# Kernel tuning notes

Measured on AMD Instinct MI355X. Metric: run time of the kernel, lower is better.

The kernel has to match this reference:

```python
import jax, jax.numpy as jnp
import numpy as np

N = 100000      # nodes
E = 1600000     # message-passing edges
P = 1000000     # prediction edges
DIN = 128       # node_in_channels
H = 128         # hidden_channels
DOUT = 64       # out_channels (node embedding)
EIN = 32        # edge_in_channels
EPS = 1e-5


def setup_inputs() -> dict:
    key = jax.random.key(0)
    ks = iter(jax.random.split(key, 48))
    nk = lambda: next(ks)
    rn = lambda shape: jax.random.normal(nk(), shape, dtype=jnp.float32)
    glorot = lambda shape: rn(shape) * (1.0 / np.sqrt(shape[-1]))
    inp = {
        "x": rn((N, DIN)),
        "edge_index": jax.random.randint(nk(), (2, E), 0, N),
        "pred_edge_index": jax.random.randint(nk(), (2, P), 0, N),
        "edge_features": rn((P, EIN)),
        # SAGEConv layer 1: lin_l (aggregated, with bias), lin_r (root, no bias)
        "sage1_Wl": glorot((H, DIN)), "sage1_bl": jnp.zeros((H,), jnp.float32), "sage1_Wr": glorot((H, DIN)),
        "bn1_g": jnp.ones((H,), jnp.float32), "bn1_b": jnp.zeros((H,), jnp.float32),
        "bn1_m": rn((H,)) * 0.1, "bn1_v": jnp.ones((H,), jnp.float32),
        # SAGEConv layer 2
        "sage2_Wl": glorot((DOUT, H)), "sage2_bl": jnp.zeros((DOUT,), jnp.float32), "sage2_Wr": glorot((DOUT, H)),
        # edge MLP: Linear(EIN, H//2) -> BN -> ReLU -> Linear(H//2, H//4)
        "edge_W1": glorot((H // 2, EIN)), "edge_b1": jnp.zeros((H // 2,), jnp.float32),
        "ebn_g": jnp.ones((H // 2,), jnp.float32), "ebn_b": jnp.zeros((H // 2,), jnp.float32),
        "ebn_m": rn((H // 2,)) * 0.1, "ebn_v": jnp.ones((H // 2,), jnp.float32),
        "edge_W2": glorot((H // 4, H // 2)), "edge_b2": jnp.zeros((H // 4,), jnp.float32),
        # predictor: Linear(2*DOUT+H//4, H) -> BN -> ReLU -> Linear(H, H//2) -> BN -> ReLU -> Linear(H//2, 1)
        "p_W1": glorot((H, 2 * DOUT + H // 4)), "p_b1": jnp.zeros((H,), jnp.float32),
        "pbn1_g": jnp.ones((H,), jnp.float32), "pbn1_b": jnp.zeros((H,), jnp.float32),
        "pbn1_m": rn((H,)) * 0.1, "pbn1_v": jnp.ones((H,), jnp.float32),
        "p_W2": glorot((H // 2, H)), "p_b2": jnp.zeros((H // 2,), jnp.float32),
        "pbn2_g": jnp.ones((H // 2,), jnp.float32), "pbn2_b": jnp.zeros((H // 2,), jnp.float32),
        "pbn2_m": rn((H // 2,)) * 0.1, "pbn2_v": jnp.ones((H // 2,), jnp.float32),
        "p_W3": glorot((1, H // 2)), "p_b3": jnp.zeros((1,), jnp.float32),
    }
    return inp


def _bn(h, g, b, m, v):
    # eval-mode BatchNorm1d with running stats
    return (h - m) * (g / jnp.sqrt(v + EPS)) + b


def _sage(h, src, dst, Wl, bl, Wr):
    # PyG SAGEConv (mean aggr): lin_l(mean of h[src] at dst) + lin_r(h)
    msg = jax.ops.segment_sum(h[src], dst, num_segments=N)        # [N, d]
    cnt = jax.ops.segment_sum(jnp.ones((src.shape[0],), h.dtype), dst, num_segments=N)
    agg = msg / jnp.maximum(cnt, 1.0)[:, None]
    return agg @ Wl.T + bl + h @ Wr.T


def reference(x, edge_index, pred_edge_index, edge_features,
              sage1_Wl, sage1_bl, sage1_Wr, bn1_g, bn1_b, bn1_m, bn1_v,
              sage2_Wl, sage2_bl, sage2_Wr,
              edge_W1, edge_b1, ebn_g, ebn_b, ebn_m, ebn_v, edge_W2, edge_b2,
              p_W1, p_b1, pbn1_g, pbn1_b, pbn1_m, pbn1_v,
              p_W2, p_b2, pbn2_g, pbn2_b, pbn2_m, pbn2_v, p_W3, p_b3):
    src, dst = edge_index[0], edge_index[1]
    # GraphSAGE encoder (eval mode: dropout off, BN running stats)
    h = _sage(x, src, dst, sage1_Wl, sage1_bl, sage1_Wr)
    h = jax.nn.relu(_bn(h, bn1_g, bn1_b, bn1_m, bn1_v))
    z = _sage(h, src, dst, sage2_Wl, sage2_bl, sage2_Wr)          # [N, DOUT]
    # edge-pair gather + concat
    combined = jnp.concatenate([z[pred_edge_index[0]], z[pred_edge_index[1]]], axis=-1)  # [P, 2*DOUT]
    # edge feature MLP
    e = edge_features @ edge_W1.T + edge_b1
    e = jax.nn.relu(_bn(e, ebn_g, ebn_b, ebn_m, ebn_v))
    e = e @ edge_W2.T + edge_b2                                   # [P, H//4]
    combined = jnp.concatenate([combined, e], axis=-1)            # [P, 2*DOUT + H//4]
    # predictor MLP
    u = combined @ p_W1.T + p_b1
    u = jax.nn.relu(_bn(u, pbn1_g, pbn1_b, pbn1_m, pbn1_v))
    u = u @ p_W2.T + p_b2
    u = jax.nn.relu(_bn(u, pbn2_g, pbn2_b, pbn2_m, pbn2_v))
    out = u @ p_W3.T + p_b3                                       # [P, 1]
    return out[:, 0]
```

## Files before the change

### kernel.cpp

```cpp
#include <hip/hip_runtime.h>

#define Nn 100000
#define Ee 1600000
#define Pp 1000000
#define EPSf 1e-5f

typedef _Float16 f16x8 __attribute__((ext_vector_type(8)));
typedef _Float16 f16x4 __attribute__((ext_vector_type(4)));
typedef _Float16 f16x2 __attribute__((ext_vector_type(2)));
typedef float f32x4 __attribute__((ext_vector_type(4)));

__device__ __forceinline__ float4 ld4(const float* p) { return *(const float4*)p; }

#define oW1l 0
#define oW1r 16384
#define oW2l 32768
#define oW2r 40960
#define oW1a 49152
#define oW1b 57344
#define oW1c 65536
#define oWe1 69632
#define oWe2 71680
#define oWp2 73728
#define W16_TOTAL 81920

#define BN_TOTAL 608

__global__ __launch_bounds__(256) void prep_kernel(
    const float* __restrict__ x,
    const float* __restrict__ s1Wl, const float* __restrict__ s1Wr,
    const float* __restrict__ s2Wl, const float* __restrict__ s2Wr,
    const float* __restrict__ pW1,  const float* __restrict__ eW1,
    const float* __restrict__ eW2,  const float* __restrict__ pW2,
    const float* __restrict__ eb1,
    const float* __restrict__ ebng, const float* __restrict__ ebnb,
    const float* __restrict__ ebnm, const float* __restrict__ ebnv,
    const float* __restrict__ eb2,
    const float* __restrict__ pb1,
    const float* __restrict__ p1g, const float* __restrict__ p1b,
    const float* __restrict__ p1m, const float* __restrict__ p1v,
    const float* __restrict__ pb2,
    const float* __restrict__ p2g, const float* __restrict__ p2b,
    const float* __restrict__ p2m, const float* __restrict__ p2v,
    const float* __restrict__ pW3,
    _Float16* __restrict__ w16, float* __restrict__ bnA,
    _Float16* __restrict__ x16) {
    int tid = blockIdx.x * 256 + threadIdx.x;
    if (tid < W16_TOTAL) {
        float v;
        if (tid < 16384)      v = s1Wl[tid];
        else if (tid < 32768) v = s1Wr[tid - 16384];
        else if (tid < 40960) v = s2Wl[tid - 32768];
        else if (tid < 49152) v = s2Wr[tid - 40960];
        else if (tid < 57344) { int l = tid - 49152; v = pW1[(l >> 6) * 160 + (l & 63)]; }
        else if (tid < 65536) { int l = tid - 57344; v = pW1[(l >> 6) * 160 + 64 + (l & 63)]; }
        else if (tid < 69632) { int l = tid - 65536; v = pW1[(l >> 5) * 160 + 128 + (l & 31)]; }
        else if (tid < 71680) v = eW1[tid - 69632];
        else if (tid < 73728) v = eW2[tid - 71680];
        else                  v = pW2[tid - 73728];
        w16[tid] = (_Float16)v;
    } else if (tid < W16_TOTAL + BN_TOTAL) {
        int b = tid - W16_TOTAL;
        float v;
        if (b < 64)       v = ebng[b] * rsqrtf(ebnv[b] + EPSf);
        else if (b < 128) { int c = b - 64;  float s = ebng[c] * rsqrtf(ebnv[c] + EPSf);
                            v = (eb1[c] - ebnm[c]) * s + ebnb[c]; }
        else if (b < 256) { int c = b - 128; v = p1g[c] * rsqrtf(p1v[c] + EPSf); }
        else if (b < 384) { int c = b - 256; float s = p1g[c] * rsqrtf(p1v[c] + EPSf);
                            v = (pb1[c] - p1m[c]) * s + p1b[c]; }
        else if (b < 448) { int c = b - 384; v = p2g[c] * rsqrtf(p2v[c] + EPSf); }
        else if (b < 512) { int c = b - 448; float s = p2g[c] * rsqrtf(p2v[c] + EPSf);
                            v = (pb2[c] - p2m[c]) * s + p2b[c]; }
        else if (b < 544) v = eb2[b - 512];
        else              v = pW3[b - 544];
        bnA[b] = v;
    }
    int stride = gridDim.x * 256;
    const int NV = Nn * 128 / 4;
    for (int i = tid; i < NV; i += stride) {
        float4 v = ((const float4*)x)[i];
        f16x4 h = {(_Float16)v.x, (_Float16)v.y, (_Float16)v.z, (_Float16)v.w};
        ((f16x4*)x16)[i] = h;
    }
}

__global__ __launch_bounds__(256) void hist_kernel(const int* __restrict__ dst,
                                                   unsigned* __restrict__ deg) {
    int i = blockIdx.x * 256 + threadIdx.x;
    if (i < Ee) atomicAdd(&deg[dst[i]], 1u);
}

__global__ __launch_bounds__(1024) void scanA_kernel(const unsigned* __restrict__ deg,
                                                     unsigned* __restrict__ escan,
                                                     unsigned* __restrict__ bsum) {
    __shared__ unsigned s[1024];
    int t = threadIdx.x;
    int gid = blockIdx.x * 1024 + t;
    unsigned v = (gid < Nn) ? deg[gid] : 0u;
    s[t] = v;
    __syncthreads();
    for (int off = 1; off < 1024; off <<= 1) {
        unsigned u = (t >= off) ? s[t - off] : 0u;
        __syncthreads();
        s[t] += u;
        __syncthreads();
    }
    if (gid < Nn) escan[gid] = s[t] - v;
    if (t == 1023) bsum[blockIdx.x] = s[1023];
}

__global__ __launch_bounds__(128) void scanB_kernel(const unsigned* __restrict__ bsum,
                                                    unsigned* __restrict__ boff,
                                                    int nblk) {
    __shared__ unsigned s[128];
    int t = threadIdx.x;
    unsigned v = (t < nblk) ? bsum[t] : 0u;
    s[t] = v;
    __syncthreads();
    for (int off = 1; off < 128; off <<= 1) {
        unsigned u = (t >= off) ? s[t - off] : 0u;
        __syncthreads();
        s[t] += u;
        __syncthreads();
    }
    if (t < nblk) boff[t] = s[t] - v;
}

__global__ __launch_bounds__(1024) void scanC_kernel(const unsigned* __restrict__ escan,
                                                     const unsigned* __restrict__ boff,
                                                     int* __restrict__ rowptr,
                                                     int* __restrict__ cursor) {
    int t = threadIdx.x;
    int gid = blockIdx.x * 1024 + t;
    if (gid < Nn) {
        int v = (int)(escan[gid] + boff[blockIdx.x]);
        rowptr[gid] = v;
        cursor[gid] = v;
    }
    if (gid == 0) rowptr[Nn] = Ee;
}

__global__ __launch_bounds__(256) void scatter_kernel(const int* __restrict__ src,
                                                      const int* __restrict__ dst,
                                                      int* __restrict__ cursor,
                                                      int* __restrict__ elist) {
    int i = blockIdx.x * 256 + threadIdx.x;
    if (i < Ee) {
        int p = atomicAdd(&cursor[dst[i]], 1);
        elist[p] = src[i];
    }
}

template<int W>
__global__ __launch_bounds__(256, 8) void aggregate16_kernel(
    const _Float16* __restrict__ feat,
    const int* __restrict__ rowptr,
    const int* __restrict__ elist,
    _Float16* __restrict__ outp) {
    int node = (blockIdx.x * 256 + threadIdx.x) >> 6;
    int lane = threadIdx.x & 63;
    if (node >= Nn) return;
    constexpr int SEGS = W / 8;
    constexpr int RPI  = 64 / SEGS;
    const int r = lane / SEGS, c = lane % SEGS;
    int beg = rowptr[node], end = rowptr[node + 1];
    int n = end - beg;
    float acc[8];
#pragma unroll
    for (int k = 0; k < 8; ++k) acc[k] = 0.f;
    for (int c0 = 0; c0 < n; c0 += 64) {
        int m = min(64, n - c0);
        int se = (lane < m) ? elist[beg + c0 + lane] : 0;
        int iters = (m + RPI - 1) / RPI;
#pragma unroll 2
        for (int i = 0; i < iters; ++i) {
            int j = i * RPI + r;
            int s = __shfl(se, j);
            if (j < m) {
                f16x8 v = *(const f16x8*)(feat + (size_t)s * W + c * 8);
#pragma unroll
                for (int k = 0; k < 8; ++k) acc[k] += (float)v[k];
            }
        }
    }
#pragma unroll
    for (int k = 0; k < 8; ++k) {
#pragma unroll
        for (int off = SEGS; off < 64; off <<= 1)
            acc[k] += __shfl_xor(acc[k], off);
    }
    if (r == 0) {
        float inv = 1.0f / fmaxf((float)n, 1.0f);
        f16x8 o;
#pragma unroll
        for (int k = 0; k < 8; ++k) o[k] = (_Float16)(acc[k] * inv);
        *(f16x8*)(outp + (size_t)node * W + c * 8) = o;
    }
}

__global__ __launch_bounds__(256) void dense1_kernel(
    const _Float16* __restrict__ A1, const _Float16* __restrict__ A2,
    const _Float16* __restrict__ W1, const _Float16* __restrict__ W2,
    const float* __restrict__ lb,
    const float* __restrict__ bng, const float* __restrict__ bnb,
    const float* __restrict__ bnm, const float* __restrict__ bnv,
    _Float16* __restrict__ out) {
    const int t = threadIdx.x;
    const int w = t >> 6, lane = t & 63;
    const int lrow = lane & 15, lq = lane >> 4;
    const int row0 = blockIdx.x * 64 + w * 16;
    const int ld = min(row0 + lrow, Nn - 1);

    f16x8 a1[4], a2[4];
#pragma unroll
    for (int i = 0; i < 4; ++i) {
        a1[i] = *(const f16x8*)(A1 + (size_t)ld * 128 + i * 32 + lq * 8);
        a2[i] = *(const f16x8*)(A2 + (size_t)ld * 128 + i * 32 + lq * 8);
    }
#pragma unroll
    for (int nt = 0; nt < 8; ++nt) {
        const _Float16* w1r = W1 + (size_t)(nt * 16 + lrow) * 128;
        const _Float16* w2r = W2 + (size_t)(nt * 16 + lrow) * 128;
        f32x4 c = {0.f, 0.f, 0.f, 0.f};
#pragma unroll
        for (int i = 0; i < 4; ++i) {
            c = __builtin_amdgcn_mfma_f32_16x16x32_f16(a1[i], *(const f16x8*)(w1r + i * 32 + lq * 8), c, 0, 0, 0);
            c = __builtin_amdgcn_mfma_f32_16x16x32_f16(a2[i], *(const f16x8*)(w2r + i * 32 + lq * 8), c, 0, 0, 0);
        }
        int cc = nt * 16 + lrow;
        float s = bng[cc] * rsqrtf(bnv[cc] + EPSf);
        float h = (lb[cc] - bnm[cc]) * s + bnb[cc];
#pragma unroll
        for (int r = 0; r < 4; ++r) {
            int gr = row0 + lq * 4 + r;
            if (gr < Nn)
                out[(size_t)gr * 128 + cc] = (_Float16)fmaxf(c[r] * s + h, 0.f);
        }
    }
}

__global__ __launch_bounds__(256) void gemmY_kernel(
    const _Float16* __restrict__ A, const _Float16* __restrict__ W,
    _Float16* __restrict__ out) {
    const int t = threadIdx.x;
    const int w = t >> 6, lane = t & 63;
    const int lrow = lane & 15, lq = lane >> 4;
    const int row0 = blockIdx.x * 64 + w * 16;
    const int ld = min(row0 + lrow, Nn - 1);
    f16x8 a[4];
#pragma unroll
    for (int i = 0; i < 4; ++i)
        a[i] = *(const f16x8*)(A + (size_t)ld * 128 + i * 32 + lq * 8);
#pragma unroll
    for (int nt = 0; nt < 4; ++nt) {
        const _Float16* wr = W + (size_t)(nt * 16 + lrow) * 128;
        f32x4 c = {0.f, 0.f, 0.f, 0.f};
#pragma unroll
        for (int i = 0; i < 4; ++i)
            c = __builtin_amdgcn_mfma_f32_16x16x32_f16(a[i], *(const f16x8*)(wr + i * 32 + lq * 8), c, 0, 0, 0);
        int cc = nt * 16 + lrow;
#pragma unroll
        for (int r = 0; r < 4; ++r) {
            int gr = row0 + lq * 4 + r;
            if (gr < Nn) out[(size_t)gr * 64 + cc] = (_Float16)c[r];
        }
    }
}

__global__ __launch_bounds__(256) void dense2b_kernel(
    const _Float16* __restrict__ aggY, const _Float16* __restrict__ A2,
    const _Float16* __restrict__ W2, const float* __restrict__ lb,
    _Float16* __restrict__ out) {
    const int t = threadIdx.x;
    const int w = t >> 6, lane = t & 63;
    const int lrow = lane & 15, lq = lane >> 4;
    const int row0 = blockIdx.x * 64 + w * 16;
    const int ld = min(row0 + lrow, Nn - 1);
    f16x8 a[4];
#pragma unroll
    for (int i = 0; i < 4; ++i)
        a[i] = *(const f16x8*)(A2 + (size_t)ld * 128 + i * 32 + lq * 8);
#pragma unroll
    for (int nt = 0; nt < 4; ++nt) {
        const _Float16* wr = W2 + (size_t)(nt * 16 + lrow) * 128;
        f32x4 c = {0.f, 0.f, 0.f, 0.f};
#pragma unroll
        for (int i = 0; i < 4; ++i)
            c = __builtin_amdgcn_mfma_f32_16x16x32_f16(a[i], *(const f16x8*)(wr + i * 32 + lq * 8), c, 0, 0, 0);
        int cc = nt * 16 + lrow;
        float b = lb[cc];
#pragma unroll
        for (int r = 0; r < 4; ++r) {
            int gr = row0 + lq * 4 + r;
            if (gr < Nn) {
                float g = (float)aggY[(size_t)gr * 64 + cc];
                out[(size_t)gr * 64 + cc] = (_Float16)(c[r] + g + b);
            }
        }
    }
}

#define EPB 128
#define NT  ((Pp + EPB - 1) / EPB)
#define EGRID 1024

#define oL_We1 0
#define oL_We2 5120
#define oL_W1a 9728
#define oL_W1b 28160
#define oL_W1c 46592
#define oL_Wp2 56832
#define oL_BN  74240
#define oL_E1  76672
#define oL_E2  95104
#define oL_ZU  105344
#define SMEM_BYTES 140160

__global__ __launch_bounds__(512, 1) void edge_kernel(
    const int* __restrict__ pe,
    const float* __restrict__ ef,
    const _Float16* __restrict__ z,
    const _Float16* __restrict__ w16,
    const float* __restrict__ bnA,
    const float* __restrict__ pb3,
    float* __restrict__ out) {
    __shared__ __align__(16) unsigned char smem[SMEM_BYTES];
    _Float16* LWe1 = (_Float16*)(smem + oL_We1);
    _Float16* LWe2 = (_Float16*)(smem + oL_We2);
    _Float16* LW1a = (_Float16*)(smem + oL_W1a);
    _Float16* LW1b = (_Float16*)(smem + oL_W1b);
    _Float16* LW1c = (_Float16*)(smem + oL_W1c);
    _Float16* LWp2 = (_Float16*)(smem + oL_Wp2);
    float*    LBN  = (float*)(smem + oL_BN);
    _Float16* E1 = (_Float16*)(smem + oL_E1);
    _Float16* E2 = (_Float16*)(smem + oL_E2);
    _Float16* ZU = (_Float16*)(smem + oL_ZU);
    _Float16* U2 = (_Float16*)(smem + oL_E1);

    const float* bn1s = LBN;        const float* bn1h = LBN + 64;
    const float* bn2s = LBN + 128;  const float* bn2h = LBN + 256;
    const float* bn3s = LBN + 384;  const float* bn3h = LBN + 448;
    const float* eb2g = LBN + 512;  const float* wp3g = LBN + 544;

    const int t = threadIdx.x;
    const int lane = t & 63;
    const int w = t >> 6;
    const int m0 = w * 16;
    const int lrow = lane & 15;
    const int lq = lane >> 4;
    const int er = lane >> 3;
    const int seg = lane & 7;
    const float pb3v = pb3[0];

    auto load_tile = [&](int tl, f16x8* Ga, f16x8* Gb, float4& Ef0, float4& Ef1) -> bool {
        if (tl >= NT) return false;
        int e0 = tl * EPB + m0;
        if (e0 >= Pp) return false;
#pragma unroll
        for (int i = 0; i < 2; ++i) {
            int eg = e0 + i * 8 + er;
            int ai = pe[eg];
            int bi = pe[Pp + eg];
            Ga[i] = *(const f16x8*)(z + (size_t)ai * 64 + seg * 8);
            Gb[i] = *(const f16x8*)(z + (size_t)bi * 64 + seg * 8);
        }
        const float* src = ef + (size_t)(e0 + lrow) * 32 + lq * 8;
        Ef0 = ld4(src); Ef1 = ld4(src + 4);
        return true;
    };

    int tile = blockIdx.x;
    f16x8 ga[2], gb[2]; float4 ef0, ef1;
    bool act = load_tile(tile, ga, gb, ef0, ef1);

    for (int u = t; u < 256; u += 512) { int r = u >> 2, s = u & 3;
        *(f16x8*)(LWe1 + r * 40 + s * 8) = *(const f16x8*)(w16 + oWe1 + r * 32 + s * 8); }
    for (int u = t; u < 256; u += 512) { int r = u >> 3, s = u & 7;
        *(f16x8*)(LWe2 + r * 72 + s * 8) = *(const f16x8*)(w16 + oWe2 + r * 64 + s * 8); }
    for (int u = t; u < 1024; u += 512) { int r = u >> 3, s = u & 7;
        *(f16x8*)(LW1a + r * 72 + s * 8) = *(const f16x8*)(w16 + oW1a + r * 64 + s * 8); }
    for (int u = t; u < 1024; u += 512) { int r = u >> 3, s = u & 7;
        *(f16x8*)(LW1b + r * 72 + s * 8) = *(const f16x8*)(w16 + oW1b + r * 64 + s * 8); }
    for (int u = t; u < 512; u += 512) { int r = u >> 2, s = u & 3;
        *(f16x8*)(LW1c + r * 40 + s * 8) = *(const f16x8*)(w16 + oW1c + r * 32 + s * 8); }
    for (int u = t; u < 1024; u += 512) { int r = u >> 4, s = u & 15;
        *(f16x8*)(LWp2 + r * 136 + s * 8) = *(const f16x8*)(w16 + oWp2 + r * 128 + s * 8); }
    for (int u = t; u < BN_TOTAL; u += 512) LBN[u] = bnA[u];
    __syncthreads();

    for (; tile < NT; tile += EGRID) {
        const int base = tile * EPB;

        if (act) {
#pragma unroll
            for (int i = 0; i < 2; ++i) {
                int e = m0 + i * 8 + er;
                *(f16x8*)(ZU + e * 136 + seg * 8) = ga[i];
                *(f16x8*)(ZU + e * 136 + 64 + seg * 8) = gb[i];
            }
        }
        f16x8 nga[2], ngb[2]; float4 nef0, nef1;
        bool nact = load_tile(tile + EGRID, nga, ngb, nef0, nef1);

        if (act) {
            {
                f16x8 a = {(_Float16)ef0.x, (_Float16)ef0.y, (_Float16)ef0.z, (_Float16)ef0.w,
                           (_Float16)ef1.x, (_Float16)ef1.y, (_Float16)ef1.z, (_Float16)ef1.w};
#pragma unroll
                for (int nt = 0; nt < 4; ++nt) {
                    f16x8 b = *(const f16x8*)(LWe1 + (nt * 16 + lrow) * 40 + lq * 8);
                    f32x4 c = {0.f, 0.f, 0.f, 0.f};
                    c = __builtin_amdgcn_mfma_f32_16x16x32_f16(a, b, c, 0, 0, 0);
                    int cc = nt * 16 + lrow;
                    float s = bn1s[cc], h = bn1h[cc];
#pragma unroll
                    for (int r = 0; r < 4; ++r) {
                        int rr = m0 + lq * 4 + r;
                        E1[rr * 72 + cc] = (_Float16)fmaxf(c[r] * s + h, 0.f);
                    }
                }
            }
            {
                f16x8 a0 = *(const f16x8*)(E1 + (m0 + lrow) * 72 + lq * 8);
                f16x8 a1 = *(const f16x8*)(E1 + (m0 + lrow) * 72 + 32 + lq * 8);
#pragma unroll
                for (int nt = 0; nt < 2; ++nt) {
                    f16x8 b0 = *(const f16x8*)(LWe2 + (nt * 16 + lrow) * 72 + lq * 8);
                    f16x8 b1 = *(const f16x8*)(LWe2 + (nt * 16 + lrow) * 72 + 32 + lq * 8);
                    f32x4 c = {0.f, 0.f, 0.f, 0.f};
                    c = __builtin_amdgcn_mfma_f32_16x16x32_f16(a0, b0, c, 0, 0, 0);
                    c = __builtin_amdgcn_mfma_f32_16x16x32_f16(a1, b1, c, 0, 0, 0);
                    int cc = nt * 16 + lrow;
                    float bias = eb2g[cc];
#pragma unroll
                    for (int r = 0; r < 4; ++r) {
                        int rr = m0 + lq * 4 + r;
                        E2[rr * 40 + cc] = (_Float16)(c[r] + bias);
                    }
                }
            }
            {
                f16x8 za0 = *(const f16x8*)(ZU + (m0 + lrow) * 136 + lq * 8);
                f16x8 za1 = *(const f16x8*)(ZU + (m0 + lrow) * 136 + 32 + lq * 8);
                f16x8 zb0 = *(const f16x8*)(ZU + (m0 + lrow) * 136 + 64 + lq * 8);
                f16x8 zb1 = *(const f16x8*)(ZU + (m0 + lrow) * 136 + 96 + lq * 8);
                f16x8 ae  = *(const f16x8*)(E2 + (m0 + lrow) * 40 + lq * 8);
#pragma unroll
                for (int nt = 0; nt < 8; ++nt) {
                    const _Float16* wa = LW1a + (nt * 16 + lrow) * 72;
                    const _Float16* wb = LW1b + (nt * 16 + lrow) * 72;
                    const _Float16* wc = LW1c + (nt * 16 + lrow) * 40;
                    f32x4 c = {0.f, 0.f, 0.f, 0.f};
                    c = __builtin_amdgcn_mfma_f32_16x16x32_f16(za0, *(const f16x8*)(wa + lq * 8),      c, 0, 0, 0);
                    c = __builtin_amdgcn_mfma_f32_16x16x32_f16(za1, *(const f16x8*)(wa + 32 + lq * 8), c, 0, 0, 0);
                    c = __builtin_amdgcn_mfma_f32_16x16x32_f16(zb0, *(const f16x8*)(wb + lq * 8),      c, 0, 0, 0);
                    c = __builtin_amdgcn_mfma_f32_16x16x32_f16(zb1, *(const f16x8*)(wb + 32 + lq * 8), c, 0, 0, 0);
                    c = __builtin_amdgcn_mfma_f32_16x16x32_f16(ae,  *(const f16x8*)(wc + lq * 8),      c, 0, 0, 0);
                    int cc = nt * 16 + lrow;
                    float s = bn2s[cc], h = bn2h[cc];
#pragma unroll
                    for (int r = 0; r < 4; ++r) {
                        int rr = m0 + lq * 4 + r;
                        ZU[rr * 136 + cc] = (_Float16)fmaxf(c[r] * s + h, 0.f);
                    }
                }
            }
            {
                f16x8 a0 = *(const f16x8*)(ZU + (m0 + lrow) * 136 + 0  + lq * 8);
                f16x8 a1 = *(const f16x8*)(ZU + (m0 + lrow) * 136 + 32 + lq * 8);
                f16x8 a2 = *(const f16x8*)(ZU + (m0 + lrow) * 136 + 64 + lq * 8);
                f16x8 a3 = *(const f16x8*)(ZU + (m0 + lrow) * 136 + 96 + lq * 8);
#pragma unroll
                for (int nt = 0; nt < 4; ++nt) {
                    const _Float16* wr = LWp2 + (nt * 16 + lrow) * 136 + lq * 8;
                    f32x4 c = {0.f, 0.f, 0.f, 0.f};
                    c = __builtin_amdgcn_mfma_f32_16x16x32_f16(a0, *(const f16x8*)(wr + 0),  c, 0, 0, 0);
                    c = __builtin_amdgcn_mfma_f32_16x16x32_f16(a1, *(const f16x8*)(wr + 32), c, 0, 0, 0);
                    c = __builtin_amdgcn_mfma_f32_16x16x32_f16(a2, *(const f16x8*)(wr + 64), c, 0, 0, 0);
                    c = __builtin_amdgcn_mfma_f32_16x16x32_f16(a3, *(const f16x8*)(wr + 96), c, 0, 0, 0);
                    int cc = nt * 16 + lrow;
                    float s = bn3s[cc], h = bn3h[cc];
#pragma unroll
                    for (int r = 0; r < 4; ++r) {
                        int rr = m0 + lq * 4 + r;
                        U2[rr * 72 + cc] = (_Float16)fmaxf(c[r] * s + h, 0.f);
                    }
                }
            }
            {
                int e = m0 + (lane >> 2);
                int c0 = (lane & 3) * 16;
                f16x8 u0 = *(const f16x8*)(U2 + e * 72 + c0);
                f16x8 u1 = *(const f16x8*)(U2 + e * 72 + c0 + 8);
                float acc = 0.f;
#pragma unroll
                for (int j = 0; j < 8; ++j) acc += (float)u0[j] * wp3g[c0 + j];
#pragma unroll
                for (int j = 0; j < 8; ++j) acc += (float)u1[j] * wp3g[c0 + 8 + j];
                acc += __shfl_xor(acc, 1);
                acc += __shfl_xor(acc, 2);
                if ((lane & 3) == 0) out[base + e] = acc + pb3v;
            }
        }
        ga[0] = nga[0]; ga[1] = nga[1];
        gb[0] = ngb[0]; gb[1] = ngb[1];
        ef0 = nef0; ef1 = nef1;
        act = nact;
    }
}

extern "C" void kernel_launch(void* const* d_in, const int* in_sizes, int n_in,
                              void* d_out, int out_size, void* d_ws, size_t ws_size,
                              hipStream_t stream) {
    const float* x    = (const float*)d_in[0];
    const int*   eidx = (const int*)d_in[1];
    const int*   pe   = (const int*)d_in[2];
    const float* ef   = (const float*)d_in[3];
    const float* s1Wl = (const float*)d_in[4];
    const float* s1bl = (const float*)d_in[5];
    const float* s1Wr = (const float*)d_in[6];
    const float* bn1g = (const float*)d_in[7];
    const float* bn1b = (const float*)d_in[8];
    const float* bn1m = (const float*)d_in[9];
    const float* bn1v = (const float*)d_in[10];
    const float* s2Wl = (const float*)d_in[11];
    const float* s2bl = (const float*)d_in[12];
    const float* s2Wr = (const float*)d_in[13];
    const float* eW1  = (const float*)d_in[14];
    const float* eb1  = (const float*)d_in[15];
    const float* ebng = (const float*)d_in[16];
    const float* ebnb = (const float*)d_in[17];
    const float* ebnm = (const float*)d_in[18];
    const float* ebnv = (const float*)d_in[19];
    const float* eW2  = (const float*)d_in[20];
    const float* eb2  = (const float*)d_in[21];
    const float* pW1  = (const float*)d_in[22];
    const float* pb1  = (const float*)d_in[23];
    const float* p1g  = (const float*)d_in[24];
    const float* p1b  = (const float*)d_in[25];
    const float* p1m  = (const float*)d_in[26];
    const float* p1v  = (const float*)d_in[27];
    const float* pW2  = (const float*)d_in[28];
    const float* pb2  = (const float*)d_in[29];
    const float* p2g  = (const float*)d_in[30];
    const float* p2b  = (const float*)d_in[31];
    const float* p2m  = (const float*)d_in[32];
    const float* p2v  = (const float*)d_in[33];
    const float* pW3  = (const float*)d_in[34];
    const float* pb3  = (const float*)d_in[35];
    float* out = (float*)d_out;

    char* wk = (char*)d_ws;
    auto carve = [&](size_t bytes) {
        char* p = wk;
        wk += (bytes + 255) & ~(size_t)255;
        return p;
    };
    unsigned*  deg    = (unsigned*)carve((size_t)Nn * 4);
    int*       rowptr = (int*)carve((size_t)(Nn + 1) * 4);
    int*       cursor = (int*)carve((size_t)Nn * 4);
    int*       elist  = (int*)carve((size_t)Ee * 4);
    unsigned*  escan  = (unsigned*)carve((size_t)Nn * 4);
    unsigned*  bsum   = (unsigned*)carve(128 * 4);
    unsigned*  boff   = (unsigned*)carve(128 * 4);
    _Float16*  w16    = (_Float16*)carve((size_t)W16_TOTAL * 2);
    float*     bnA    = (float*)carve((size_t)BN_TOTAL * 4);
    _Float16*  bufX   = (_Float16*)carve((size_t)Nn * 128 * 2);
    _Float16*  bufA   = (_Float16*)carve((size_t)Nn * 128 * 2);
    _Float16*  bufH   = (_Float16*)carve((size_t)Nn * 128 * 2);
    _Float16*  bufY   = bufX;
    _Float16*  bufZ   = bufX + (size_t)Nn * 64;
    _Float16*  bufAy  = bufA;

    const int* e_src = eidx;
    const int* e_dst = eidx + Ee;
    const int SBLK = (Nn + 1023) / 1024;

    hipMemsetAsync(deg, 0, (size_t)Nn * 4, stream);
    prep_kernel<<<800, 256, 0, stream>>>(x, s1Wl, s1Wr, s2Wl, s2Wr, pW1, eW1, eW2, pW2,
                                         eb1, ebng, ebnb, ebnm, ebnv, eb2,
                                         pb1, p1g, p1b, p1m, p1v,
                                         pb2, p2g, p2b, p2m, p2v, pW3,
                                         w16, bnA, bufX);
    hist_kernel<<<(Ee + 255) / 256, 256, 0, stream>>>(e_dst, deg);
    scanA_kernel<<<SBLK, 1024, 0, stream>>>(deg, escan, bsum);
    scanB_kernel<<<1, 128, 0, stream>>>(bsum, boff, SBLK);
    scanC_kernel<<<SBLK, 1024, 0, stream>>>(escan, boff, rowptr, cursor);
    scatter_kernel<<<(Ee + 255) / 256, 256, 0, stream>>>(e_src, e_dst, cursor, elist);

    aggregate16_kernel<128><<<Nn / 4, 256, 0, stream>>>(bufX, rowptr, elist, bufA);
    dense1_kernel<<<(Nn + 63) / 64, 256, 0, stream>>>(
        bufA, bufX, w16 + oW1l, w16 + oW1r, s1bl, bn1g, bn1b, bn1m, bn1v, bufH);

    gemmY_kernel<<<(Nn + 63) / 64, 256, 0, stream>>>(bufH, w16 + oW2l, bufY);
    aggregate16_kernel<64><<<Nn / 4, 256, 0, stream>>>(bufY, rowptr, elist, bufAy);
    dense2b_kernel<<<(Nn + 63) / 64, 256, 0, stream>>>(
        bufAy, bufH, w16 + oW2r, s2bl, bufZ);

    edge_kernel<<<EGRID, 512, 0, stream>>>(pe, ef, bufZ, w16, bnA, pb3, out);
}
```

Baseline: 799.1 us.

## Keep predictor W1 weights in registers, transpose MFMA outputs, fuse final dot

Moves the W1a/W1b predictor weight fragments out of LDS into per-thread registers loaded once, shrinking shared memory enough to raise launch bounds to two blocks per CU. It swaps MFMA operand order so each lane's outputs are contiguous columns, which allows vectorized f16x4 LDS stores and float4 BN parameter loads. The last layer's output is reduced directly into the final dot product with p_W3, dropping the U2 staging buffer and a pass over LDS. MFMA sections are wrapped in s_setprio. Holding 32 f16x8 weight vectors per thread raises register pressure, which could cause spills at the two-block occupancy target.

```diff
diff --git a/kernel.cpp b/kernel.cpp
--- a/kernel.cpp
+++ b/kernel.cpp
@@ -306,17 +306,15 @@
 
 #define oL_We1 0
 #define oL_We2 5120
-#define oL_W1a 9728
-#define oL_W1b 28160
-#define oL_W1c 46592
-#define oL_Wp2 56832
-#define oL_BN  74240
-#define oL_E1  76672
-#define oL_E2  95104
-#define oL_ZU  105344
-#define SMEM_BYTES 140160
-
-__global__ __launch_bounds__(512, 1) void edge_kernel(
+#define oL_W1c 9728
+#define oL_Wp2 19968
+#define oL_BN  37376
+#define oL_E1  39808
+#define oL_E2  58240
+#define oL_ZU  68480
+#define SMEM_BYTES 103296
+
+__global__ __launch_bounds__(512, 2) void edge_kernel(
     const int* __restrict__ pe,
     const float* __restrict__ ef,
     const _Float16* __restrict__ z,
@@ -327,15 +325,12 @@
     __shared__ __align__(16) unsigned char smem[SMEM_BYTES];
     _Float16* LWe1 = (_Float16*)(smem + oL_We1);
     _Float16* LWe2 = (_Float16*)(smem + oL_We2);
-    _Float16* LW1a = (_Float16*)(smem + oL_W1a);
-    _Float16* LW1b = (_Float16*)(smem + oL_W1b);
     _Float16* LW1c = (_Float16*)(smem + oL_W1c);
     _Float16* LWp2 = (_Float16*)(smem + oL_Wp2);
     float*    LBN  = (float*)(smem + oL_BN);
     _Float16* E1 = (_Float16*)(smem + oL_E1);
     _Float16* E2 = (_Float16*)(smem + oL_E2);
     _Float16* ZU = (_Float16*)(smem + oL_ZU);
-    _Float16* U2 = (_Float16*)(smem + oL_E1);
 
     const float* bn1s = LBN;        const float* bn1h = LBN + 64;
     const float* bn2s = LBN + 128;  const float* bn2h = LBN + 256;
@@ -373,14 +368,21 @@
     f16x8 ga[2], gb[2]; float4 ef0, ef1;
     bool act = load_tile(tile, ga, gb, ef0, ef1);
 
+    f16x8 wa0[8], wa1[8], wb0[8], wb1[8];
+#pragma unroll
+    for (int nt = 0; nt < 8; ++nt) {
+        const _Float16* ra = w16 + oW1a + (size_t)(nt * 16 + lrow) * 64;
+        const _Float16* rb = w16 + oW1b + (size_t)(nt * 16 + lrow) * 64;
+        wa0[nt] = *(const f16x8*)(ra + lq * 8);
+        wa1[nt] = *(const f16x8*)(ra + 32 + lq * 8);
+        wb0[nt] = *(const f16x8*)(rb + lq * 8);
+        wb1[nt] = *(const f16x8*)(rb + 32 + lq * 8);
+    }
+
     for (int u = t; u < 256; u += 512) { int r = u >> 2, s = u & 3;
         *(f16x8*)(LWe1 + r * 40 + s * 8) = *(const f16x8*)(w16 + oWe1 + r * 32 + s * 8); }
     for (int u = t; u < 256; u += 512) { int r = u >> 3, s = u & 7;
         *(f16x8*)(LWe2 + r * 72 + s * 8) = *(const f16x8*)(w16 + oWe2 + r * 64 + s * 8); }
-    for (int u = t; u < 1024; u += 512) { int r = u >> 3, s = u & 7;
-        *(f16x8*)(LW1a + r * 72 + s * 8) = *(const f16x8*)(w16 + oW1a + r * 64 + s * 8); }
-    for (int u = t; u < 1024; u += 512) { int r = u >> 3, s = u & 7;
-        *(f16x8*)(LW1b + r * 72 + s * 8) = *(const f16x8*)(w16 + oW1b + r * 64 + s * 8); }
     for (int u = t; u < 512; u += 512) { int r = u >> 2, s = u & 3;
         *(f16x8*)(LW1c + r * 40 + s * 8) = *(const f16x8*)(w16 + oW1c + r * 32 + s * 8); }
     for (int u = t; u < 1024; u += 512) { int r = u >> 4, s = u & 15;
@@ -403,103 +405,104 @@
         bool nact = load_tile(tile + EGRID, nga, ngb, nef0, nef1);
 
         if (act) {
+            const int erow = m0 + lrow;
             {
-                f16x8 a = {(_Float16)ef0.x, (_Float16)ef0.y, (_Float16)ef0.z, (_Float16)ef0.w,
+                f16x8 b = {(_Float16)ef0.x, (_Float16)ef0.y, (_Float16)ef0.z, (_Float16)ef0.w,
                            (_Float16)ef1.x, (_Float16)ef1.y, (_Float16)ef1.z, (_Float16)ef1.w};
 #pragma unroll
                 for (int nt = 0; nt < 4; ++nt) {
-                    f16x8 b = *(const f16x8*)(LWe1 + (nt * 16 + lrow) * 40 + lq * 8);
+                    f16x8 wf = *(const f16x8*)(LWe1 + (nt * 16 + lrow) * 40 + lq * 8);
                     f32x4 c = {0.f, 0.f, 0.f, 0.f};
-                    c = __builtin_amdgcn_mfma_f32_16x16x32_f16(a, b, c, 0, 0, 0);
-                    int cc = nt * 16 + lrow;
-                    float s = bn1s[cc], h = bn1h[cc];
-#pragma unroll
-                    for (int r = 0; r < 4; ++r) {
-                        int rr = m0 + lq * 4 + r;
-                        E1[rr * 72 + cc] = (_Float16)fmaxf(c[r] * s + h, 0.f);
-                    }
+                    c = __builtin_amdgcn_mfma_f32_16x16x32_f16(wf, b, c, 0, 0, 0);
+                    int cb = nt * 16 + lq * 4;
+                    float4 s = *(const float4*)(bn1s + cb);
+                    float4 h = *(const float4*)(bn1h + cb);
+                    f16x4 o;
+                    o[0] = (_Float16)fmaxf(c[0] * s.x + h.x, 0.f);
+                    o[1] = (_Float16)fmaxf(c[1] * s.y + h.y, 0.f);
+                    o[2] = (_Float16)fmaxf(c[2] * s.z + h.z, 0.f);
+                    o[3] = (_Float16)fmaxf(c[3] * s.w + h.w, 0.f);
+                    *(f16x4*)(E1 + erow * 72 + cb) = o;
                 }
             }
             {
-                f16x8 a0 = *(const f16x8*)(E1 + (m0 + lrow) * 72 + lq * 8);
-                f16x8 a1 = *(const f16x8*)(E1 + (m0 + lrow) * 72 + 32 + lq * 8);
+                f16x8 a0 = *(const f16x8*)(E1 + erow * 72 + lq * 8);
+                f16x8 a1 = *(const f16x8*)(E1 + erow * 72 + 32 + lq * 8);
 #pragma unroll
                 for (int nt = 0; nt < 2; ++nt) {
                     f16x8 b0 = *(const f16x8*)(LWe2 + (nt * 16 + lrow) * 72 + lq * 8);
                     f16x8 b1 = *(const f16x8*)(LWe2 + (nt * 16 + lrow) * 72 + 32 + lq * 8);
                     f32x4 c = {0.f, 0.f, 0.f, 0.f};
-                    c = __builtin_amdgcn_mfma_f32_16x16x32_f16(a0, b0, c, 0, 0, 0);
-                    c = __builtin_amdgcn_mfma_f32_16x16x32_f16(a1, b1, c, 0, 0, 0);
-                    int cc = nt * 16 + lrow;
-                    float bias = eb2g[cc];
-#pragma unroll
-                    for (int r = 0; r < 4; ++r) {
-                        int rr = m0 + lq * 4 + r;
-                        E2[rr * 40 + cc] = (_Float16)(c[r] + bias);
-                    }
+                    c = __builtin_amdgcn_mfma_f32_16x16x32_f16(b0, a0, c, 0, 0, 0);
+                    c = __builtin_amdgcn_mfma_f32_16x16x32_f16(b1, a1, c, 0, 0, 0);
+                    int cb = nt * 16 + lq * 4;
+                    float4 bias = *(const float4*)(eb2g + cb);
+                    f16x4 o;
+                    o[0] = (_Float16)(c[0] + bias.x);
+                    o[1] = (_Float16)(c[1] + bias.y);
+                    o[2] = (_Float16)(c[2] + bias.z);
+                    o[3] = (_Float16)(c[3] + bias.w);
+                    *(f16x4*)(E2 + erow * 40 + cb) = o;
                 }
             }
             {
-                f16x8 za0 = *(const f16x8*)(ZU + (m0 + lrow) * 136 + lq * 8);
-                f16x8 za1 = *(const f16x8*)(ZU + (m0 + lrow) * 136 + 32 + lq * 8);
-                f16x8 zb0 = *(const f16x8*)(ZU + (m0 + lrow) * 136 + 64 + lq * 8);
-                f16x8 zb1 = *(const f16x8*)(ZU + (m0 + lrow) * 136 + 96 + lq * 8);
-                f16x8 ae  = *(const f16x8*)(E2 + (m0 + lrow) * 40 + lq * 8);
+                const int zr = erow * 136;
+                f16x8 za0 = *(const f16x8*)(ZU + zr + lq * 8);
+                f16x8 za1 = *(const f16x8*)(ZU + zr + 32 + lq * 8);
+                f16x8 zb0 = *(const f16x8*)(ZU + zr + 64 + lq * 8);
+                f16x8 zb1 = *(const f16x8*)(ZU + zr + 96 + lq * 8);
+                f16x8 ae  = *(const f16x8*)(E2 + erow * 40 + lq * 8);
+                __builtin_amdgcn_s_setprio(1);
 #pragma unroll
                 for (int nt = 0; nt < 8; ++nt) {
-                    const _Float16* wa = LW1a + (nt * 16 + lrow) * 72;
-                    const _Float16* wb = LW1b + (nt * 16 + lrow) * 72;
-                    const _Float16* wc = LW1c + (nt * 16 + lrow) * 40;
+                    f16x8 wc = *(const f16x8*)(LW1c + (nt * 16 + lrow) * 40 + lq * 8);
                     f32x4 c = {0.f, 0.f, 0.f, 0.f};
-                    c = __builtin_amdgcn_mfma_f32_16x16x32_f16(za0, *(const f16x8*)(wa + lq * 8),      c, 0, 0, 0);
-                    c = __builtin_amdgcn_mfma_f32_16x16x32_f16(za1, *(const f16x8*)(wa + 32 + lq * 8), c, 0, 0, 0);
-                    c = __builtin_amdgcn_mfma_f32_16x16x32_f16(zb0, *(const f16x8*)(wb + lq * 8),      c, 0, 0, 0);
-                    c = __builtin_amdgcn_mfma_f32_16x16x32_f16(zb1, *(const f16x8*)(wb + 32 + lq * 8), c, 0, 0, 0);
-                    c = __builtin_amdgcn_mfma_f32_16x16x32_f16(ae,  *(const f16x8*)(wc + lq * 8),      c, 0, 0, 0);
-                    int cc = nt * 16 + lrow;
-                    float s = bn2s[cc], h = bn2h[cc];
-#pragma unroll
-                    for (int r = 0; r < 4; ++r) {
-                        int rr = m0 + lq * 4 + r;
-                        ZU[rr * 136 + cc] = (_Float16)fmaxf(c[r] * s + h, 0.f);
-                    }
+                    c = __builtin_amdgcn_mfma_f32_16x16x32_f16(wa0[nt], za0, c, 0, 0, 0);
+                    c = __builtin_amdgcn_mfma_f32_16x16x32_f16(wa1[nt], za1, c, 0, 0, 0);
+                    c = __builtin_amdgcn_mfma_f32_16x16x32_f16(wb0[nt], zb0, c, 0, 0, 0);
+                    c = __builtin_amdgcn_mfma_f32_16x16x32_f16(wb1[nt], zb1, c, 0, 0, 0);
+                    c = __builtin_amdgcn_mfma_f32_16x16x32_f16(wc,      ae,  c, 0, 0, 0);
+                    int cb = nt * 16 + lq * 4;
+                    float4 s = *(const float4*)(bn2s + cb);
+                    float4 h = *(const float4*)(bn2h + cb);
+                    f16x4 o;
+                    o[0] = (_Float16)fmaxf(c[0] * s.x + h.x, 0.f);
+                    o[1] = (_Float16)fmaxf(c[1] * s.y + h.y, 0.f);
+                    o[2] = (_Float16)fmaxf(c[2] * s.z + h.z, 0.f);
+                    o[3] = (_Float16)fmaxf(c[3] * s.w + h.w, 0.f);
+                    *(f16x4*)(ZU + zr + cb) = o;
                 }
+                __builtin_amdgcn_s_setprio(0);
             }
             {
-                f16x8 a0 = *(const f16x8*)(ZU + (m0 + lrow) * 136 + 0  + lq * 8);
-                f16x8 a1 = *(const f16x8*)(ZU + (m0 + lrow) * 136 + 32 + lq * 8);
-                f16x8 a2 = *(const f16x8*)(ZU + (m0 + lrow) * 136 + 64 + lq * 8);
-                f16x8 a3 = *(const f16x8*)(ZU + (m0 + lrow) * 136 + 96 + lq * 8);
+                const int zr = erow * 136;
+                f16x8 a0 = *(const f16x8*)(ZU + zr + 0  + lq * 8);
+                f16x8 a1 = *(const f16x8*)(ZU + zr + 32 + lq * 8);
+                f16x8 a2 = *(const f16x8*)(ZU + zr + 64 + lq * 8);
+                f16x8 a3 = *(const f16x8*)(ZU + zr + 96 + lq * 8);
+                float acc = 0.f;
+                __builtin_amdgcn_s_setprio(1);
 #pragma unroll
                 for (int nt = 0; nt < 4; ++nt) {
                     const _Float16* wr = LWp2 + (nt * 16 + lrow) * 136 + lq * 8;
                     f32x4 c = {0.f, 0.f, 0.f, 0.f};
-                    c = __builtin_amdgcn_mfma_f32_16x16x32_f16(a0, *(const f16x8*)(wr + 0),  c, 0, 0, 0);
-                    c = __builtin_amdgcn_mfma_f32_16x16x32_f16(a1, *(const f16x8*)(wr + 32), c, 0, 0, 0);
-                    c = __builtin_amdgcn_mfma_f32_16x16x32_f16(a2, *(const f16x8*)(wr + 64), c, 0, 0, 0);
-                    c = __builtin_amdgcn_mfma_f32_16x16x32_f16(a3, *(const f16x8*)(wr + 96), c, 0, 0, 0);
-                    int cc = nt * 16 + lrow;
-                    float s = bn3s[cc], h = bn3h[cc];
-#pragma unroll
-                    for (int r = 0; r < 4; ++r) {
-                        int rr = m0 + lq * 4 + r;
-                        U2[rr * 72 + cc] = (_Float16)fmaxf(c[r] * s + h, 0.f);
-                    }
+                    c = __builtin_amdgcn_mfma_f32_16x16x32_f16(*(const f16x8*)(wr + 0),  a0, c, 0, 0, 0);
+                    c = __builtin_amdgcn_mfma_f32_16x16x32_f16(*(const f16x8*)(wr + 32), a1, c, 0, 0, 0);
+                    c = __builtin_amdgcn_mfma_f32_16x16x32_f16(*(const f16x8*)(wr + 64), a2, c, 0, 0, 0);
+                    c = __builtin_amdgcn_mfma_f32_16x16x32_f16(*(const f16x8*)(wr + 96), a3, c, 0, 0, 0);
+                    int cb = nt * 16 + lq * 4;
+                    float4 s  = *(const float4*)(bn3s + cb);
+                    float4 h  = *(const float4*)(bn3h + cb);
+                    float4 w3 = *(const float4*)(wp3g + cb);
+                    acc += fmaxf(c[0] * s.x + h.x, 0.f) * w3.x;
+                    acc += fmaxf(c[1] * s.y + h.y, 0.f) * w3.y;
+                    acc += fmaxf(c[2] * s.z + h.z, 0.f) * w3.z;
+                    acc += fmaxf(c[3] * s.w + h.w, 0.f) * w3.w;
                 }
-            }
-            {
-                int e = m0 + (lane >> 2);
-                int c0 = (lane & 3) * 16;
-                f16x8 u0 = *(const f16x8*)(U2 + e * 72 + c0);
-                f16x8 u1 = *(const f16x8*)(U2 + e * 72 + c0 + 8);
-                float acc = 0.f;
-#pragma unroll
-                for (int j = 0; j < 8; ++j) acc += (float)u0[j] * wp3g[c0 + j];
-#pragma unroll
-                for (int j = 0; j < 8; ++j) acc += (float)u1[j] * wp3g[c0 + 8 + j];
-                acc += __shfl_xor(acc, 1);
-                acc += __shfl_xor(acc, 2);
-                if ((lane & 3) == 0) out[base + e] = acc + pb3v;
+                __builtin_amdgcn_s_setprio(0);
+                acc += __shfl_xor(acc, 16);
+                acc += __shfl_xor(acc, 32);
+                if (lane < 16) out[base + m0 + lane] = acc + pb3v;
             }
         }
         ga[0] = nga[0]; ga[1] = nga[1];
```

Measured after the change: 766.7 us. 1.04x faster.
